# Kernel tuning notes

Hardware: AMD Instinct MI355X
Metric: run time of the kernel (lower is better)

Reference implementation:

```python
import jax, jax.numpy as jnp
import numpy as np

B = 65536      # batch
HID = 128      # hidden_dim
Q = 4          # IRK stages
DT = 0.1       # default time step
N_ITERS = 10   # fixed-point iterations


def setup_inputs() -> dict:
    key = jax.random.key(0)
    ks = jax.random.split(key, 16)
    def lin(k, fan_in, fan_out):
        return jax.random.normal(k, (fan_in, fan_out), jnp.float32) / np.sqrt(fan_in)
    return {
        "X0": jax.random.normal(ks[0], (B, 4), jnp.float32),
        "W1": lin(ks[1], 4, HID),   "b1": jnp.zeros((HID,), jnp.float32),
        "W2": lin(ks[2], HID, HID), "b2": jnp.zeros((HID,), jnp.float32),
        "W3": lin(ks[3], HID, HID), "b3": jnp.zeros((HID,), jnp.float32),
        "W4": lin(ks[4], HID, 4),   "b4": jnp.zeros((4,), jnp.float32),
        "lam1": jax.random.normal(ks[5], (1,), jnp.float32) * 0.1 + 0.5,
        "lam2": jax.random.normal(ks[6], (1,), jnp.float32) * 0.1 + 0.5,
        "lam3": jax.random.normal(ks[7], (1,), jnp.float32) * 0.1 + 0.5,
        "lam4": jax.random.normal(ks[8], (1,), jnp.float32) * 0.1 + 0.5,
        "IRK_alpha": jax.random.normal(ks[9], (Q, Q), jnp.float32) * 0.25,
        "IRK_beta": jax.random.normal(ks[10], (Q,), jnp.float32) * 0.25,
    }


def reference(X0, W1, b1, W2, b2, W3, b3, W4, b4,
              lam1, lam2, lam3, lam4, IRK_alpha, IRK_beta):
    dt = DT

    def mlp(x):  # (N,4) -> (N,4)
        h = jnp.tanh(x @ W1 + b1)
        h = jnp.tanh(h @ W2 + b2)
        h = jnp.tanh(h @ W3 + b3)
        return h @ W4 + b4

    def hamiltonian_vf(x):  # x: (N,4) = [p1,p2,q1,q2]
        H_out = mlp(x)
        dp_dt = -lam1 * H_out[:, 2:] - lam2 * x[:, 2:]
        dq_dt = lam3 * H_out[:, :2] + lam4 * x[:, :2]
        return jnp.concatenate([dp_dt, dq_dt], axis=1)

    bsz = X0.shape[0]
    K = jnp.zeros((bsz, Q, 4), X0.dtype)
    for _ in range(N_ITERS):  # small fixed trip count, unrolled
        # same contraction as original torch einsum 'bqi,ij->bqj'
        X_stages = X0[:, None, :] + dt * jnp.einsum('bqi,ij->bqj', K, IRK_alpha)
        K = hamiltonian_vf(X_stages.reshape(-1, 4)).reshape(bsz, Q, 4)

    # intended IRK final combine: X1 = X0 + dt * sum_q beta_q K[:,q,:]
    X1 = X0 + dt * jnp.einsum('bqi,q->bi', K, IRK_beta)
    return X1
```

## Files before the change

### kernel.cpp

```cpp
#include <hip/hip_runtime.h>
#include <hip/hip_bf16.h>
#include <stdint.h>

#define HID    128
#define DT     0.1f
#define NITER  10
#define NTHR   512
#define NW     8
#define NBLK   512
#define NCH    2
#define SCALE  2.885390081777927f

typedef __attribute__((ext_vector_type(8))) short bf16x8;
typedef __attribute__((ext_vector_type(4))) float f32x4;
typedef __attribute__((ext_vector_type(2))) unsigned int u32x2;
typedef __attribute__((ext_vector_type(4))) unsigned int u32x4;

union FragU { bf16x8 v; uint32_t u[4]; };

struct alignas(16) Smem {
    uint32_t w2f[8 * 4 * 64 * 4];
    uint32_t w3f[8 * 4 * 64 * 4];
    uint32_t w1c[8 * 16 * 2];
    uint32_t w4l[4 * 64 * 4];
    float    b1[HID], b2[HID], b3[HID];
    float    kk[NW * 32 * 4];
};

__device__ __forceinline__ uint16_t f2bf(float f) {
    uint32_t u = __float_as_uint(f);
    return (uint16_t)((u + 0x7fffu + ((u >> 16) & 1u)) >> 16);
}

__device__ __forceinline__ uint32_t pk2(float a, float b) {
    __hip_bfloat162 h = __float22bfloat162_rn(float2{a, b});
    return *reinterpret_cast<uint32_t*>(&h);
}

__device__ __forceinline__ f32x4 tanh4(f32x4 y) {
    float e0 = __builtin_amdgcn_exp2f(fminf(y[0], 30.f)) + 1.0f;
    float e1 = __builtin_amdgcn_exp2f(fminf(y[1], 30.f)) + 1.0f;
    float e2 = __builtin_amdgcn_exp2f(fminf(y[2], 30.f)) + 1.0f;
    float e3 = __builtin_amdgcn_exp2f(fminf(y[3], 30.f)) + 1.0f;
    float p01   = e0 * e1;
    float p012  = p01 * e2;
    float p0123 = p012 * e3;
    float r     = __builtin_amdgcn_rcpf(p0123);
    float i3   = p012 * r;
    float r012 = e3 * r;
    float i2   = p01 * r012;
    float r01  = e2 * r012;
    float i1   = e0 * r01;
    float i0   = e1 * r01;
    return (f32x4){fmaf(-2.f, i0, 1.f), fmaf(-2.f, i1, 1.f),
                   fmaf(-2.f, i2, 1.f), fmaf(-2.f, i3, 1.f)};
}

__device__ __forceinline__ float uread(const float* p) {
    return __uint_as_float(__builtin_amdgcn_readfirstlane(__float_as_uint(*p)));
}

__device__ __forceinline__ bf16x8 pack2(const f32x4& a0, const f32x4& a1) {
    f32x4 t0 = tanh4(a0);
    f32x4 t1 = tanh4(a1);
    FragU f;
    f.u[0] = pk2(t0[0], t0[1]);
    f.u[1] = pk2(t0[2], t0[3]);
    f.u[2] = pk2(t1[0], t1[1]);
    f.u[3] = pk2(t1[2], t1[3]);
    return f.v;
}

__device__ __forceinline__ void dense_reg(
    const uint32_t* __restrict__ wf, const float* __restrict__ bias,
    bf16x8 (&bfrA)[4], bf16x8 (&bfrB)[4], int lane, int g, uint32_t zz)
{
    bf16x8 nA[4], nB[4];
    #pragma unroll
    for (int op = 0; op < 4; ++op) {
        f32x4 b0 = *(const f32x4*)&bias[(2 * op) * 16 + 4 * g + zz];
        f32x4 b1 = *(const f32x4*)&bias[(2 * op + 1) * 16 + 4 * g + zz];
        f32x4 a0A = b0, a0B = b0, a1A = b1, a1B = b1;
        __builtin_amdgcn_s_setprio(1);
        #pragma unroll
        for (int kt = 0; kt < 4; ++kt) {
            bf16x8 w0 = *(const bf16x8*)&wf[(((2 * op) * 4 + kt) * 64 + lane) * 4 + zz];
            a0A = __builtin_amdgcn_mfma_f32_16x16x32_bf16(w0, bfrA[kt], a0A, 0, 0, 0);
            a0B = __builtin_amdgcn_mfma_f32_16x16x32_bf16(w0, bfrB[kt], a0B, 0, 0, 0);
        }
        #pragma unroll
        for (int kt = 0; kt < 4; ++kt) {
            bf16x8 w1 = *(const bf16x8*)&wf[(((2 * op + 1) * 4 + kt) * 64 + lane) * 4 + zz];
            a1A = __builtin_amdgcn_mfma_f32_16x16x32_bf16(w1, bfrA[kt], a1A, 0, 0, 0);
            a1B = __builtin_amdgcn_mfma_f32_16x16x32_bf16(w1, bfrB[kt], a1B, 0, 0, 0);
        }
        __builtin_amdgcn_s_setprio(0);
        nA[op] = pack2(a0A, a1A);
        nB[op] = pack2(a0B, a1B);
    }
    #pragma unroll
    for (int kt = 0; kt < 4; ++kt) { bfrA[kt] = nA[kt]; bfrB[kt] = nB[kt]; }
}

__global__ __launch_bounds__(NTHR, 1) void pinn_irk_reg(
    const float* __restrict__ x0g,
    const float* __restrict__ w1g, const float* __restrict__ b1g,
    const float* __restrict__ w2g, const float* __restrict__ b2g,
    const float* __restrict__ w3g, const float* __restrict__ b3g,
    const float* __restrict__ w4g, const float* __restrict__ b4g,
    const float* __restrict__ l1g, const float* __restrict__ l2g,
    const float* __restrict__ l3g, const float* __restrict__ l4g,
    const float* __restrict__ alg, const float* __restrict__ beg,
    float* __restrict__ outg)
{
    __shared__ Smem S;
    const int t    = threadIdx.x;
    const int blk  = blockIdx.x;
    const int lane = t & 63;
    const int w    = t >> 6;
    const int ln   = lane & 15;
    const int g    = lane >> 4;
    const bool owner = (g == 0);

    const float L0 = uread(l1g), L1v = uread(l2g), L2v = uread(l3g), L3v = uread(l4g);
    const float B40 = uread(b4g), B41 = uread(b4g + 1);
    const float B42 = uread(b4g + 2), B43 = uread(b4g + 3);
    const float BE0 = uread(beg), BE1 = uread(beg + 1);
    const float BE2 = uread(beg + 2), BE3 = uread(beg + 3);
    float A[16];
    #pragma unroll
    for (int i = 0; i < 16; ++i) A[i] = uread(alg + i);

    for (int s = t; s < 2048; s += NTHR) {
        int lane_s = s & 63, kto = s >> 6;
        int kt = kto & 3, ot = kto >> 2;
        int m = ot * 16 + (lane_s & 15), gs = lane_s >> 4;
        uint32_t f2[4], f3[4];
        #pragma unroll
        for (int jj = 0; jj < 4; ++jj) {
            int k = 16 * (2 * kt + (jj >> 1)) + 4 * gs + 2 * (jj & 1);
            f2[jj] = (uint32_t)f2bf(w2g[k * HID + m] * SCALE)
                   | ((uint32_t)f2bf(w2g[(k + 1) * HID + m] * SCALE) << 16);
            f3[jj] = (uint32_t)f2bf(w3g[k * HID + m] * SCALE)
                   | ((uint32_t)f2bf(w3g[(k + 1) * HID + m] * SCALE) << 16);
        }
        *(u32x4*)&S.w2f[s * 4] = (u32x4){f2[0], f2[1], f2[2], f2[3]};
        *(u32x4*)&S.w3f[s * 4] = (u32x4){f3[0], f3[1], f3[2], f3[3]};
    }
    if (t < 128) {
        int ot = t >> 4, lns = t & 15;
        int m = ot * 16 + lns;
        S.w1c[t * 2]     = (uint32_t)f2bf(w1g[0 * HID + m] * SCALE)
                         | ((uint32_t)f2bf(w1g[1 * HID + m] * SCALE) << 16);
        S.w1c[t * 2 + 1] = (uint32_t)f2bf(w1g[2 * HID + m] * SCALE)
                         | ((uint32_t)f2bf(w1g[3 * HID + m] * SCALE) << 16);
    }
    if (t < 256) {
        int lane_s = t & 63, kt = t >> 6;
        int lns = lane_s & 15, gs = lane_s >> 4;
        uint32_t f[4];
        #pragma unroll
        for (int jj = 0; jj < 4; ++jj) {
            int k0 = 16 * (2 * kt + (jj >> 1)) + 4 * gs + 2 * (jj & 1);
            uint32_t lo = (lns < 4) ? (uint32_t)f2bf(w4g[k0 * 4 + lns]) : 0u;
            uint32_t hi = (lns < 4) ? (uint32_t)f2bf(w4g[(k0 + 1) * 4 + lns]) : 0u;
            f[jj] = lo | (hi << 16);
        }
        *(u32x4*)&S.w4l[t * 4] = (u32x4){f[0], f[1], f[2], f[3]};
    }
    if (t < HID) {
        S.b1[t] = b1g[t] * SCALE;
        S.b2[t] = b2g[t] * SCALE;
        S.b3[t] = b3g[t] * SCALE;
    }
    __syncthreads();

    for (int ch = 0; ch < NCH; ++ch) {
        const int base = ((blk * NW + w) * NCH + ch) * 32;
        f32x4 XA0 = *(const f32x4*)&x0g[((base + ln) >> 2) * 4];
        f32x4 XB0 = *(const f32x4*)&x0g[((base + 16 + ln) >> 2) * 4];
        f32x4 XA = XA0, XB = XB0;
        float* kkw = &S.kk[w * 128];

        #pragma unroll 1
        for (int it = 0; it < NITER; ++it) {
            uint32_t zz = 0;
            asm volatile("" : "+v"(zz));
            zz &= ~3u;

            FragU xa, xb;
            xa.u[0] = owner ? pk2(XA[0], XA[1]) : 0u;
            xa.u[1] = owner ? pk2(XA[2], XA[3]) : 0u;
            xa.u[2] = 0u; xa.u[3] = 0u;
            xb.u[0] = owner ? pk2(XB[0], XB[1]) : 0u;
            xb.u[1] = owner ? pk2(XB[2], XB[3]) : 0u;
            xb.u[2] = 0u; xb.u[3] = 0u;

            bf16x8 bfrA[4], bfrB[4];
            #pragma unroll
            for (int op = 0; op < 4; ++op) {
                f32x4 b0 = *(const f32x4*)&S.b1[(2 * op) * 16 + 4 * g + zz];
                f32x4 b1 = *(const f32x4*)&S.b1[(2 * op + 1) * 16 + 4 * g + zz];
                u32x2 c0 = *(const u32x2*)&S.w1c[((2 * op) * 16 + ln) * 2 + zz];
                u32x2 c1 = *(const u32x2*)&S.w1c[((2 * op + 1) * 16 + ln) * 2 + zz];
                FragU w0f, w1f;
                w0f.u[0] = owner ? c0.x : 0u; w0f.u[1] = owner ? c0.y : 0u;
                w0f.u[2] = 0u; w0f.u[3] = 0u;
                w1f.u[0] = owner ? c1.x : 0u; w1f.u[1] = owner ? c1.y : 0u;
                w1f.u[2] = 0u; w1f.u[3] = 0u;
                f32x4 a0A = __builtin_amdgcn_mfma_f32_16x16x32_bf16(w0f.v, xa.v, b0, 0, 0, 0);
                f32x4 a0B = __builtin_amdgcn_mfma_f32_16x16x32_bf16(w0f.v, xb.v, b0, 0, 0, 0);
                f32x4 a1A = __builtin_amdgcn_mfma_f32_16x16x32_bf16(w1f.v, xa.v, b1, 0, 0, 0);
                f32x4 a1B = __builtin_amdgcn_mfma_f32_16x16x32_bf16(w1f.v, xb.v, b1, 0, 0, 0);
                bfrA[op] = pack2(a0A, a1A);
                bfrB[op] = pack2(a0B, a1B);
            }

            dense_reg(S.w2f, S.b2, bfrA, bfrB, lane, g, zz);
            dense_reg(S.w3f, S.b3, bfrA, bfrB, lane, g, zz);

            f32x4 kA = {0.f, 0.f, 0.f, 0.f}, kB = {0.f, 0.f, 0.f, 0.f};
            __builtin_amdgcn_s_setprio(1);
            #pragma unroll
            for (int kt = 0; kt < 4; ++kt) {
                bf16x8 wfr = *(const bf16x8*)&S.w4l[(kt * 64 + lane) * 4 + zz];
                kA = __builtin_amdgcn_mfma_f32_16x16x32_bf16(wfr, bfrA[kt], kA, 0, 0, 0);
                kB = __builtin_amdgcn_mfma_f32_16x16x32_bf16(wfr, bfrB[kt], kB, 0, 0, 0);
            }
            __builtin_amdgcn_s_setprio(0);
            {
                float h0 = kA[0] + B40, h1 = kA[1] + B41;
                float h2 = kA[2] + B42, h3 = kA[3] + B43;
                f32x4 kvA = (f32x4){-L0 * h2 - L1v * XA[2], -L0 * h3 - L1v * XA[3],
                                     L2v * h0 + L3v * XA[0],  L2v * h1 + L3v * XA[1]};
                h0 = kB[0] + B40; h1 = kB[1] + B41;
                h2 = kB[2] + B42; h3 = kB[3] + B43;
                f32x4 kvB = (f32x4){-L0 * h2 - L1v * XB[2], -L0 * h3 - L1v * XB[3],
                                     L2v * h0 + L3v * XB[0],  L2v * h1 + L3v * XB[1]};
                if (owner) {
                    *(f32x4*)&kkw[ln * 4]        = kvA;
                    *(f32x4*)&kkw[(16 + ln) * 4] = kvB;
                }
                #pragma unroll
                for (int c = 0; c < 4; ++c) {
                    float sA = kvA[0] * A[c] + kvA[1] * A[4 + c]
                             + kvA[2] * A[8 + c] + kvA[3] * A[12 + c];
                    float sB = kvB[0] * A[c] + kvB[1] * A[4 + c]
                             + kvB[2] * A[8 + c] + kvB[3] * A[12 + c];
                    XA[c] = fmaf(DT, sA, XA0[c]);
                    XB[c] = fmaf(DT, sB, XB0[c]);
                }
            }
        }

        if (lane < 32) {
            int bl_ = lane >> 2, i = lane & 3;
            float s = BE0 * kkw[(bl_ * 4 + 0) * 4 + i]
                    + BE1 * kkw[(bl_ * 4 + 1) * 4 + i]
                    + BE2 * kkw[(bl_ * 4 + 2) * 4 + i]
                    + BE3 * kkw[(bl_ * 4 + 3) * 4 + i];
            int idx = base + lane;
            outg[idx] = x0g[idx] + DT * s;
        }
    }
}

extern "C" void kernel_launch(void* const* d_in, const int* in_sizes, int n_in,
                              void* d_out, int out_size, void* d_ws, size_t ws_size,
                              hipStream_t stream) {
    (void)in_sizes; (void)n_in; (void)d_ws; (void)ws_size; (void)out_size;

    dim3 grid(NBLK);
    dim3 block(NTHR);

    pinn_irk_reg<<<grid, block, 0, stream>>>(
        (const float*)d_in[0],
        (const float*)d_in[1],  (const float*)d_in[2],
        (const float*)d_in[3],  (const float*)d_in[4],
        (const float*)d_in[5],  (const float*)d_in[6],
        (const float*)d_in[7],  (const float*)d_in[8],
        (const float*)d_in[9],  (const float*)d_in[10],
        (const float*)d_in[11], (const float*)d_in[12],
        (const float*)d_in[13], (const float*)d_in[14],
        (float*)d_out);
}
```

Before: 435.0 us.

## Double warps per block with one chunk each, simplify tanh to per-element rcp

Blocks grow to 1024 threads (16 waves), and each wave now handles one chunk of rows instead of two, so more waves are resident and can hide latency. The batched tanh, which shared a single reciprocal across four values, is replaced by a per-element exp2 plus reciprocal. This removes the clamp and the long serial multiply chain but issues four reciprocals per group instead of one. Dropping the clamp relies on exp2 overflowing to inf so that rcp returns 0, and fewer rows per wave lowers instruction-level parallelism.

```diff
diff --git a/kernel.cpp b/kernel.cpp
--- a/kernel.cpp
+++ b/kernel.cpp
@@ -5,10 +5,10 @@
 #define HID    128
 #define DT     0.1f
 #define NITER  10
-#define NTHR   512
-#define NW     8
+#define NTHR   1024
+#define NW     16
 #define NBLK   512
-#define NCH    2
+#define NCH    1
 #define SCALE  2.885390081777927f
 
 typedef __attribute__((ext_vector_type(8))) short bf16x8;
@@ -37,23 +37,9 @@
     return *reinterpret_cast<uint32_t*>(&h);
 }
 
-__device__ __forceinline__ f32x4 tanh4(f32x4 y) {
-    float e0 = __builtin_amdgcn_exp2f(fminf(y[0], 30.f)) + 1.0f;
-    float e1 = __builtin_amdgcn_exp2f(fminf(y[1], 30.f)) + 1.0f;
-    float e2 = __builtin_amdgcn_exp2f(fminf(y[2], 30.f)) + 1.0f;
-    float e3 = __builtin_amdgcn_exp2f(fminf(y[3], 30.f)) + 1.0f;
-    float p01   = e0 * e1;
-    float p012  = p01 * e2;
-    float p0123 = p012 * e3;
-    float r     = __builtin_amdgcn_rcpf(p0123);
-    float i3   = p012 * r;
-    float r012 = e3 * r;
-    float i2   = p01 * r012;
-    float r01  = e2 * r012;
-    float i1   = e0 * r01;
-    float i0   = e1 * r01;
-    return (f32x4){fmaf(-2.f, i0, 1.f), fmaf(-2.f, i1, 1.f),
-                   fmaf(-2.f, i2, 1.f), fmaf(-2.f, i3, 1.f)};
+__device__ __forceinline__ float tanh_pre(float y) {
+    float e = __builtin_amdgcn_exp2f(y);
+    return fmaf(-2.0f, __builtin_amdgcn_rcpf(e + 1.0f), 1.0f);
 }
 
 __device__ __forceinline__ float uread(const float* p) {
@@ -61,13 +47,11 @@
 }
 
 __device__ __forceinline__ bf16x8 pack2(const f32x4& a0, const f32x4& a1) {
-    f32x4 t0 = tanh4(a0);
-    f32x4 t1 = tanh4(a1);
     FragU f;
-    f.u[0] = pk2(t0[0], t0[1]);
-    f.u[1] = pk2(t0[2], t0[3]);
-    f.u[2] = pk2(t1[0], t1[1]);
-    f.u[3] = pk2(t1[2], t1[3]);
+    f.u[0] = pk2(tanh_pre(a0[0]), tanh_pre(a0[1]));
+    f.u[1] = pk2(tanh_pre(a0[2]), tanh_pre(a0[3]));
+    f.u[2] = pk2(tanh_pre(a1[0]), tanh_pre(a1[1]));
+    f.u[3] = pk2(tanh_pre(a1[2]), tanh_pre(a1[3]));
     return f.v;
 }
 
```

After: 362.2 us. 1.2x faster.
